# Performance work log

Measured on AMD Instinct MI355X. Metric: run time of the kernel, lower is better.

Reference implementation:

```python
import jax, jax.numpy as jnp
import numpy as np

EMB_DIM = 512
CATE1_CNT = 10
VOCAB = 100000
H_D = 1024
BN_EPS = 1e-5
NEG = -1e30  # masked value for max-pool


def setup_inputs() -> dict:
    key = jax.random.key(0)
    ks = jax.random.split(key, 12)
    B, LT, LD = 1024, 50, 200
    title = jax.random.randint(ks[0], (B, LT), 0, VOCAB, dtype=jnp.int64)
    desc = jax.random.randint(ks[1], (B, LD), 0, VOCAB, dtype=jnp.int64)
    t_len = jax.random.randint(ks[2], (B,), 1, LT + 1, dtype=jnp.int64)
    d_len = jax.random.randint(ks[3], (B,), 1, LD + 1, dtype=jnp.int64)
    emb = jax.random.normal(ks[4], (VOCAB, EMB_DIM), dtype=jnp.float32) * 0.02
    W_fc = jax.random.normal(ks[5], (4 * EMB_DIM, H_D), dtype=jnp.float32) * (1.0 / np.sqrt(4 * EMB_DIM))
    b_fc = jnp.zeros((H_D,), dtype=jnp.float32)
    gamma = jnp.ones((H_D,), dtype=jnp.float32)
    beta = jnp.zeros((H_D,), dtype=jnp.float32)
    W_clf = jax.random.normal(ks[6], (H_D, CATE1_CNT), dtype=jnp.float32) * (1.0 / np.sqrt(H_D))
    b_clf = jnp.zeros((CATE1_CNT,), dtype=jnp.float32)
    return {"title": title, "desc": desc, "t_len": t_len, "d_len": d_len,
            "emb": emb, "W_fc": W_fc, "b_fc": b_fc, "gamma": gamma,
            "beta": beta, "W_clf": W_clf, "b_clf": b_clf}


def _swem_pool(tokens, lens, emb):
    # tokens: [B, L] int, lens: [B] int -> (avg, max) each [B, D]
    e = emb[tokens]                                   # [B, L, D] gather
    L = tokens.shape[1]
    mask = (jnp.arange(L)[None, :] < lens[:, None])[..., None]  # [B, L, 1]
    s = jnp.sum(jnp.where(mask, e, 0.0), axis=1)      # [B, D]
    avg = s / jnp.maximum(lens, 1).astype(e.dtype)[:, None]
    mx = jnp.max(jnp.where(mask, e, NEG), axis=1)     # [B, D]
    return avg, mx


def reference(title, desc, t_len, d_len, emb, W_fc, b_fc, gamma, beta, W_clf, b_clf):
    t_avg, t_max = _swem_pool(title, t_len, emb)
    d_avg, d_max = _swem_pool(desc, d_len, emb)
    swem = jnp.concatenate([t_avg, t_max, d_avg, d_max], axis=-1)  # [B, 2048]
    h = swem @ W_fc + b_fc                                         # [B, H_D]
    # BatchNorm1d in training mode: batch statistics
    mean = jnp.mean(h, axis=0)
    var = jnp.var(h, axis=0)
    h = (h - mean) * jax.lax.rsqrt(var + BN_EPS) * gamma + beta
    h = jax.nn.relu(h)
    return h @ W_clf + b_clf                                       # [B, 10]
```

## Files before the change

### kernel.cpp

```cpp
#include <hip/hip_runtime.h>
#include <hip/hip_bf16.h>

#define EMB_DIM 512
#define B_SZ 1024
#define LT 50
#define LD 200
#define H_D 1024
#define K_FC 2048
#define NCLS 10
#define BN_EPS 1e-5f
#define NEGV -1e30f

typedef short short8 __attribute__((ext_vector_type(8)));
typedef float f32x4 __attribute__((ext_vector_type(4)));

#define SWZ(r, b) ((b) ^ (((r) & 7) << 4))

#define ACC4(S, M, E) \
  S.x += E.x; S.y += E.y; S.z += E.z; S.w += E.w; \
  M.x = fmaxf(M.x, E.x); M.y = fmaxf(M.y, E.y); \
  M.z = fmaxf(M.z, E.z); M.w = fmaxf(M.w, E.w);

__global__ __launch_bounds__(512) void pool_tr_kernel(
    const int* __restrict__ title, const int* __restrict__ desc,
    const int* __restrict__ t_len, const int* __restrict__ d_len,
    const float* __restrict__ emb, __hip_bfloat16* __restrict__ swem,
    const float* __restrict__ W, __hip_bfloat16* __restrict__ Wt) {
  __shared__ float sm[8192];
  __shared__ int idxs[264];

  const int bid = blockIdx.x;
  const int tid = threadIdx.x;

  if (bid >= 2 * B_SZ) {
    const int t = bid - 2 * B_SZ;
    const int n0 = (t & 15) * 64;
    const int k0 = (t >> 4) * 64;
#pragma unroll
    for (int i = 0; i < 8; ++i) {
      int idx = i * 512 + tid;
      int r = idx >> 6, c = idx & 63;
      sm[r * 65 + c] = W[(size_t)(k0 + r) * H_D + n0 + c];
    }
    __syncthreads();
#pragma unroll
    for (int i = 0; i < 8; ++i) {
      int idx = i * 512 + tid;
      int r = idx >> 6, c = idx & 63;
      Wt[(size_t)(n0 + r) * K_FC + k0 + c] = __float2bfloat16(sm[c * 65 + r]);
    }
    return;
  }

  const int b = bid >> 1;
  const int half = bid & 1;
  const int wave = tid >> 6;
  const int lane = tid & 63;
  const int dbase = half * 256 + lane * 4;

  if (tid < LT) idxs[tid] = title[b * LT + tid];
  else if (tid >= 64 && tid < 64 + LD) idxs[tid] = desc[b * LD + tid - 64];
  const int tl = t_len[b];
  const int dl = d_len[b];
  __syncthreads();

#define POOL_LIST(LEN, IDXOFF, SARR, MARR)                                         \
  {                                                                                \
    float4 s0 = make_float4(0.f, 0.f, 0.f, 0.f), s1 = s0;                          \
    float4 m0 = make_float4(NEGV, NEGV, NEGV, NEGV), m1 = m0;                      \
    const int cnt = (LEN > wave) ? ((LEN - wave + 7) >> 3) : 0;                    \
    if (cnt >= 2) {                                                                \
      float4 e0 = *reinterpret_cast<const float4*>(                                \
          emb + (size_t)idxs[IDXOFF + wave] * EMB_DIM + dbase);                    \
      float4 e1 = *reinterpret_cast<const float4*>(                                \
          emb + (size_t)idxs[IDXOFF + wave + 8] * EMB_DIM + dbase);                \
      int i = 2;                                                                   \
      for (; i + 1 < cnt; i += 2) {                                                \
        float4 n0 = *reinterpret_cast<const float4*>(                              \
            emb + (size_t)idxs[IDXOFF + wave + i * 8] * EMB_DIM + dbase);          \
        float4 n1 = *reinterpret_cast<const float4*>(                              \
            emb + (size_t)idxs[IDXOFF + wave + (i + 1) * 8] * EMB_DIM + dbase);    \
        ACC4(s0, m0, e0); ACC4(s1, m1, e1);                                        \
        e0 = n0; e1 = n1;                                                          \
      }                                                                            \
      ACC4(s0, m0, e0); ACC4(s1, m1, e1);                                          \
      if (i < cnt) {                                                               \
        float4 t2 = *reinterpret_cast<const float4*>(                              \
            emb + (size_t)idxs[IDXOFF + wave + i * 8] * EMB_DIM + dbase);          \
        ACC4(s0, m0, t2);                                                          \
      }                                                                            \
    } else if (cnt == 1) {                                                         \
      float4 e0 = *reinterpret_cast<const float4*>(                                \
          emb + (size_t)idxs[IDXOFF + wave] * EMB_DIM + dbase);                    \
      ACC4(s0, m0, e0);                                                            \
    }                                                                              \
    s0.x += s1.x; s0.y += s1.y; s0.z += s1.z; s0.w += s1.w;                        \
    m0.x = fmaxf(m0.x, m1.x); m0.y = fmaxf(m0.y, m1.y);                            \
    m0.z = fmaxf(m0.z, m1.z); m0.w = fmaxf(m0.w, m1.w);                            \
    *reinterpret_cast<float4*>(&sm[(SARR * 8 + wave) * 256 + lane * 4]) = s0;      \
    *reinterpret_cast<float4*>(&sm[(MARR * 8 + wave) * 256 + lane * 4]) = m0;      \
  }

  POOL_LIST(tl, 0, 0, 1)
  POOL_LIST(dl, 64, 2, 3)

  __syncthreads();

  if (tid < 64) {
    const float it = 1.0f / (float)tl;
    const float id = 1.0f / (float)dl;
    float4 ts = make_float4(0.f, 0.f, 0.f, 0.f);
    float4 tm = make_float4(NEGV, NEGV, NEGV, NEGV);
    float4 ds = make_float4(0.f, 0.f, 0.f, 0.f);
    float4 dm = make_float4(NEGV, NEGV, NEGV, NEGV);
#pragma unroll
    for (int w = 0; w < 8; ++w) {
      float4 a = *reinterpret_cast<const float4*>(&sm[(0 * 8 + w) * 256 + tid * 4]);
      ts.x += a.x; ts.y += a.y; ts.z += a.z; ts.w += a.w;
      float4 bmx = *reinterpret_cast<const float4*>(&sm[(1 * 8 + w) * 256 + tid * 4]);
      tm.x = fmaxf(tm.x, bmx.x); tm.y = fmaxf(tm.y, bmx.y);
      tm.z = fmaxf(tm.z, bmx.z); tm.w = fmaxf(tm.w, bmx.w);
      float4 c = *reinterpret_cast<const float4*>(&sm[(2 * 8 + w) * 256 + tid * 4]);
      ds.x += c.x; ds.y += c.y; ds.z += c.z; ds.w += c.w;
      float4 dmx = *reinterpret_cast<const float4*>(&sm[(3 * 8 + w) * 256 + tid * 4]);
      dm.x = fmaxf(dm.x, dmx.x); dm.y = fmaxf(dm.y, dmx.y);
      dm.z = fmaxf(dm.z, dmx.z); dm.w = fmaxf(dm.w, dmx.w);
    }
    __hip_bfloat16* row = swem + (size_t)b * K_FC + half * 256 + tid * 4;
    union { ushort4 v; __hip_bfloat16 h[4]; } u;
    u.h[0] = __float2bfloat16(ts.x * it); u.h[1] = __float2bfloat16(ts.y * it);
    u.h[2] = __float2bfloat16(ts.z * it); u.h[3] = __float2bfloat16(ts.w * it);
    *reinterpret_cast<ushort4*>(&row[0 * EMB_DIM]) = u.v;
    u.h[0] = __float2bfloat16(tm.x); u.h[1] = __float2bfloat16(tm.y);
    u.h[2] = __float2bfloat16(tm.z); u.h[3] = __float2bfloat16(tm.w);
    *reinterpret_cast<ushort4*>(&row[1 * EMB_DIM]) = u.v;
    u.h[0] = __float2bfloat16(ds.x * id); u.h[1] = __float2bfloat16(ds.y * id);
    u.h[2] = __float2bfloat16(ds.z * id); u.h[3] = __float2bfloat16(ds.w * id);
    *reinterpret_cast<ushort4*>(&row[2 * EMB_DIM]) = u.v;
    u.h[0] = __float2bfloat16(dm.x); u.h[1] = __float2bfloat16(dm.y);
    u.h[2] = __float2bfloat16(dm.z); u.h[3] = __float2bfloat16(dm.w);
    *reinterpret_cast<ushort4*>(&row[3 * EMB_DIM]) = u.v;
  }
}

__global__ __launch_bounds__(256) void gemm_mfma_kernel(
    const __hip_bfloat16* __restrict__ A,
    const __hip_bfloat16* __restrict__ Bt,
    const float* __restrict__ bias, float* __restrict__ C,
    float* __restrict__ psum, float* __restrict__ psq) {
  __shared__ unsigned char As[8192];
  __shared__ unsigned char Bs[8192];
  __shared__ float reds[2][2][2][16];
  __shared__ float redq[2][2][2][16];
  const int tid = threadIdx.x;
  const int lane = tid & 63;
  const int wave = tid >> 6;
  const int wr = wave >> 1, wc = wave & 1;
  const int m0 = blockIdx.y * 64, n0 = blockIdx.x * 64;

  f32x4 acc[2][2] = {};

  const int c0 = tid * 2, c1 = tid * 2 + 1;
  const int r0s = c0 >> 3, o0 = c0 & 7;
  const int r1s = c1 >> 3, o1 = c1 & 7;
  const int hi = lane >> 4;
  const int lo = lane & 15;

  for (int k0 = 0; k0 < K_FC; k0 += 64) {
    float4 a0 = *reinterpret_cast<const float4*>(A + (size_t)(m0 + r0s) * K_FC + k0 + o0 * 8);
    float4 a1 = *reinterpret_cast<const float4*>(A + (size_t)(m0 + r1s) * K_FC + k0 + o1 * 8);
    float4 b0 = *reinterpret_cast<const float4*>(Bt + (size_t)(n0 + r0s) * K_FC + k0 + o0 * 8);
    float4 b1 = *reinterpret_cast<const float4*>(Bt + (size_t)(n0 + r1s) * K_FC + k0 + o1 * 8);
    __syncthreads();
    *reinterpret_cast<float4*>(As + SWZ(r0s, r0s * 128 + o0 * 16)) = a0;
    *reinterpret_cast<float4*>(As + SWZ(r1s, r1s * 128 + o1 * 16)) = a1;
    *reinterpret_cast<float4*>(Bs + SWZ(r0s, r0s * 128 + o0 * 16)) = b0;
    *reinterpret_cast<float4*>(Bs + SWZ(r1s, r1s * 128 + o1 * 16)) = b1;
    __syncthreads();

#pragma unroll
    for (int kks = 0; kks < 2; ++kks) {
      short8 af[2], bfr[2];
#pragma unroll
      for (int mi = 0; mi < 2; ++mi) {
        int r = wr * 32 + mi * 16 + lo;
        af[mi] = *reinterpret_cast<const short8*>(As + SWZ(r, r * 128 + kks * 64 + hi * 16));
      }
#pragma unroll
      for (int ni = 0; ni < 2; ++ni) {
        int r = wc * 32 + ni * 16 + lo;
        bfr[ni] = *reinterpret_cast<const short8*>(Bs + SWZ(r, r * 128 + kks * 64 + hi * 16));
      }
#pragma unroll
      for (int mi = 0; mi < 2; ++mi)
#pragma unroll
        for (int ni = 0; ni < 2; ++ni)
          acc[mi][ni] = __builtin_amdgcn_mfma_f32_16x16x32_bf16(af[mi], bfr[ni], acc[mi][ni], 0, 0, 0);
    }
  }

#pragma unroll
  for (int ni = 0; ni < 2; ++ni) {
    int col = n0 + wc * 32 + ni * 16 + lo;
    float bv = bias[col];
    float s = 0.f, q = 0.f;
#pragma unroll
    for (int mi = 0; mi < 2; ++mi) {
#pragma unroll
      for (int r = 0; r < 4; ++r) {
        float v = acc[mi][ni][r] + bv;
        s += v; q += v * v;
        int rowm = m0 + wr * 32 + mi * 16 + hi * 4 + r;
        C[(size_t)rowm * H_D + col] = v;
      }
    }
    s += __shfl_xor(s, 16);
    s += __shfl_xor(s, 32);
    q += __shfl_xor(q, 16);
    q += __shfl_xor(q, 32);
    if (lane < 16) { reds[wr][wc][ni][lo] = s; redq[wr][wc][ni][lo] = q; }
  }
  __syncthreads();
  if (tid < 64) {
    int wc2 = tid >> 5, ni2 = (tid >> 4) & 1, lo2 = tid & 15;
    float s = reds[0][wc2][ni2][lo2] + reds[1][wc2][ni2][lo2];
    float q = redq[0][wc2][ni2][lo2] + redq[1][wc2][ni2][lo2];
    psum[blockIdx.y * H_D + n0 + tid] = s;
    psq[blockIdx.y * H_D + n0 + tid] = q;
  }
}

__global__ __launch_bounds__(256) void bn_final_kernel(
    const float* __restrict__ psum, const float* __restrict__ psq,
    const float* __restrict__ gamma, const float* __restrict__ beta,
    float* __restrict__ scale, float* __restrict__ shift) {
  const int col = blockIdx.x * 256 + threadIdx.x;
  float s = 0.f, q = 0.f;
#pragma unroll
  for (int i = 0; i < 16; ++i) {
    s += psum[i * H_D + col];
    q += psq[i * H_D + col];
  }
  const float inv_n = 1.0f / (float)B_SZ;
  float mean = s * inv_n;
  float var = q * inv_n - mean * mean;
  float rstd = rsqrtf(var + BN_EPS);
  float sc = rstd * gamma[col];
  scale[col] = sc;
  shift[col] = beta[col] - mean * sc;
}

__global__ __launch_bounds__(256) void clf_kernel(
    const float* __restrict__ h, const float* __restrict__ scale,
    const float* __restrict__ shift, const float* __restrict__ W,
    const float* __restrict__ bclf, float* __restrict__ out) {
  const int row = blockIdx.x;
  const int tid = threadIdx.x;
  float acc[NCLS] = {};
  for (int k = tid; k < H_D; k += 256) {
    float v = h[(size_t)row * H_D + k] * scale[k] + shift[k];
    v = fmaxf(v, 0.f);
    const float* w = &W[(size_t)k * NCLS];
#pragma unroll
    for (int j = 0; j < NCLS; ++j) acc[j] += v * w[j];
  }
#pragma unroll
  for (int j = 0; j < NCLS; ++j) {
    float v = acc[j];
#pragma unroll
    for (int off = 32; off > 0; off >>= 1) v += __shfl_down(v, off, 64);
    acc[j] = v;
  }
  __shared__ float part[4][NCLS];
  const int wave = tid >> 6;
  const int lane = tid & 63;
  if (lane == 0) {
#pragma unroll
    for (int j = 0; j < NCLS; ++j) part[wave][j] = acc[j];
  }
  __syncthreads();
  if (tid < NCLS) {
    float s = part[0][tid] + part[1][tid] + part[2][tid] + part[3][tid] + bclf[tid];
    out[(size_t)row * NCLS + tid] = s;
  }
}

extern "C" void kernel_launch(void* const* d_in, const int* in_sizes, int n_in,
                              void* d_out, int out_size, void* d_ws, size_t ws_size,
                              hipStream_t stream) {
  const int* title = (const int*)d_in[0];
  const int* desc  = (const int*)d_in[1];
  const int* t_len = (const int*)d_in[2];
  const int* d_len = (const int*)d_in[3];
  const float* emb   = (const float*)d_in[4];
  const float* W_fc  = (const float*)d_in[5];
  const float* b_fc  = (const float*)d_in[6];
  const float* gamma = (const float*)d_in[7];
  const float* beta  = (const float*)d_in[8];
  const float* W_clf = (const float*)d_in[9];
  const float* b_clf = (const float*)d_in[10];
  float* out = (float*)d_out;

  unsigned char* ws = (unsigned char*)d_ws;
  __hip_bfloat16* swem = (__hip_bfloat16*)ws;
  __hip_bfloat16* Wt   = (__hip_bfloat16*)(ws + (4u << 20));
  float* h     = (float*)(ws + (8u << 20));
  float* psum  = (float*)(ws + (12u << 20));
  float* psq   = psum + 16 * H_D;
  float* scale = psq + 16 * H_D;
  float* shift = scale + H_D;

  const int n_tr_blocks = (K_FC / 64) * (H_D / 64);
  pool_tr_kernel<<<2 * B_SZ + n_tr_blocks, 512, 0, stream>>>(
      title, desc, t_len, d_len, emb, swem, W_fc, Wt);
  gemm_mfma_kernel<<<dim3(H_D / 64, B_SZ / 64), 256, 0, stream>>>(swem, Wt, b_fc, h, psum, psq);
  bn_final_kernel<<<H_D / 256, 256, 0, stream>>>(psum, psq, gamma, beta, scale, shift);
  clf_kernel<<<B_SZ, 256, 0, stream>>>(h, scale, shift, W_clf, b_clf, out);
}
```

Measured before the change: 77.80 us.

## Register-prefetch next GEMM tile and transpose classifier weights for coalesced dot

The GEMM main loop now issues global loads for the next K-tile into registers right after the LDS store barrier, so the loads overlap the MFMA work on the current tile instead of stalling at the start of each iteration. Separately, the classifier weight is transposed once by an extra block in the pool/transpose kernel. The classifier kernel now stages the ReLU'd activations in shared memory and has each wave compute whole class dot products with coalesced weight reads. This removes the strided 10-wide weight reads and the ten-way shuffle reduction, at the cost of an extra block and slightly more register pressure in the GEMM.

```diff
diff --git a/kernel.cpp b/kernel.cpp
--- a/kernel.cpp
+++ b/kernel.cpp
@@ -25,7 +25,8 @@
     const int* __restrict__ title, const int* __restrict__ desc,
     const int* __restrict__ t_len, const int* __restrict__ d_len,
     const float* __restrict__ emb, __hip_bfloat16* __restrict__ swem,
-    const float* __restrict__ W, __hip_bfloat16* __restrict__ Wt) {
+    const float* __restrict__ W, __hip_bfloat16* __restrict__ Wt,
+    const float* __restrict__ Wclf, float* __restrict__ WclfT) {
   __shared__ float sm[8192];
   __shared__ int idxs[264];
 
@@ -34,6 +35,13 @@
 
   if (bid >= 2 * B_SZ) {
     const int t = bid - 2 * B_SZ;
+    if (t == 512) {
+      for (int idx = tid; idx < NCLS * H_D; idx += 512) {
+        int j = idx >> 10, k = idx & 1023;
+        WclfT[j * H_D + k] = Wclf[(size_t)k * NCLS + j];
+      }
+      return;
+    }
     const int n0 = (t & 15) * 64;
     const int k0 = (t >> 4) * 64;
 #pragma unroll
@@ -166,17 +174,30 @@
   const int hi = lane >> 4;
   const int lo = lane & 15;
 
+  const __hip_bfloat16* pa0 = A + (size_t)(m0 + r0s) * K_FC + o0 * 8;
+  const __hip_bfloat16* pa1 = A + (size_t)(m0 + r1s) * K_FC + o1 * 8;
+  const __hip_bfloat16* pb0 = Bt + (size_t)(n0 + r0s) * K_FC + o0 * 8;
+  const __hip_bfloat16* pb1 = Bt + (size_t)(n0 + r1s) * K_FC + o1 * 8;
+
+  float4 a0 = *reinterpret_cast<const float4*>(pa0);
+  float4 a1 = *reinterpret_cast<const float4*>(pa1);
+  float4 b0 = *reinterpret_cast<const float4*>(pb0);
+  float4 b1 = *reinterpret_cast<const float4*>(pb1);
+
   for (int k0 = 0; k0 < K_FC; k0 += 64) {
-    float4 a0 = *reinterpret_cast<const float4*>(A + (size_t)(m0 + r0s) * K_FC + k0 + o0 * 8);
-    float4 a1 = *reinterpret_cast<const float4*>(A + (size_t)(m0 + r1s) * K_FC + k0 + o1 * 8);
-    float4 b0 = *reinterpret_cast<const float4*>(Bt + (size_t)(n0 + r0s) * K_FC + k0 + o0 * 8);
-    float4 b1 = *reinterpret_cast<const float4*>(Bt + (size_t)(n0 + r1s) * K_FC + k0 + o1 * 8);
     __syncthreads();
     *reinterpret_cast<float4*>(As + SWZ(r0s, r0s * 128 + o0 * 16)) = a0;
     *reinterpret_cast<float4*>(As + SWZ(r1s, r1s * 128 + o1 * 16)) = a1;
     *reinterpret_cast<float4*>(Bs + SWZ(r0s, r0s * 128 + o0 * 16)) = b0;
     *reinterpret_cast<float4*>(Bs + SWZ(r1s, r1s * 128 + o1 * 16)) = b1;
     __syncthreads();
+
+    if (k0 + 64 < K_FC) {
+      a0 = *reinterpret_cast<const float4*>(pa0 + k0 + 64);
+      a1 = *reinterpret_cast<const float4*>(pa1 + k0 + 64);
+      b0 = *reinterpret_cast<const float4*>(pb0 + k0 + 64);
+      b1 = *reinterpret_cast<const float4*>(pb1 + k0 + 64);
+    }
 
 #pragma unroll
     for (int kks = 0; kks < 2; ++kks) {
@@ -252,36 +273,30 @@
 
 __global__ __launch_bounds__(256) void clf_kernel(
     const float* __restrict__ h, const float* __restrict__ scale,
-    const float* __restrict__ shift, const float* __restrict__ W,
+    const float* __restrict__ shift, const float* __restrict__ WT,
     const float* __restrict__ bclf, float* __restrict__ out) {
+  __shared__ float v[H_D];
   const int row = blockIdx.x;
   const int tid = threadIdx.x;
-  float acc[NCLS] = {};
-  for (int k = tid; k < H_D; k += 256) {
-    float v = h[(size_t)row * H_D + k] * scale[k] + shift[k];
-    v = fmaxf(v, 0.f);
-    const float* w = &W[(size_t)k * NCLS];
-#pragma unroll
-    for (int j = 0; j < NCLS; ++j) acc[j] += v * w[j];
-  }
-#pragma unroll
-  for (int j = 0; j < NCLS; ++j) {
-    float v = acc[j];
-#pragma unroll
-    for (int off = 32; off > 0; off >>= 1) v += __shfl_down(v, off, 64);
-    acc[j] = v;
-  }
-  __shared__ float part[4][NCLS];
-  const int wave = tid >> 6;
-  const int lane = tid & 63;
-  if (lane == 0) {
-#pragma unroll
-    for (int j = 0; j < NCLS; ++j) part[wave][j] = acc[j];
+#pragma unroll
+  for (int i = 0; i < 4; ++i) {
+    int k = tid + i * 256;
+    float x = h[(size_t)row * H_D + k] * scale[k] + shift[k];
+    v[k] = fmaxf(x, 0.f);
   }
   __syncthreads();
-  if (tid < NCLS) {
-    float s = part[0][tid] + part[1][tid] + part[2][tid] + part[3][tid] + bclf[tid];
-    out[(size_t)row * NCLS + tid] = s;
+  const int wave = tid >> 6, lane = tid & 63;
+  for (int j = wave; j < NCLS; j += 4) {
+    const float* wrow = WT + j * H_D;
+    float acc = 0.f;
+#pragma unroll
+    for (int i = 0; i < 16; ++i) {
+      int k = lane + i * 64;
+      acc += v[k] * wrow[k];
+    }
+#pragma unroll
+    for (int off = 32; off > 0; off >>= 1) acc += __shfl_down(acc, off, 64);
+    if (lane == 0) out[(size_t)row * NCLS + j] = acc + bclf[j];
   }
 }
 
@@ -309,11 +324,12 @@
   float* psq   = psum + 16 * H_D;
   float* scale = psq + 16 * H_D;
   float* shift = scale + H_D;
-
-  const int n_tr_blocks = (K_FC / 64) * (H_D / 64);
+  float* WclfT = shift + H_D;
+
+  const int n_tr_blocks = (K_FC / 64) * (H_D / 64) + 1;
   pool_tr_kernel<<<2 * B_SZ + n_tr_blocks, 512, 0, stream>>>(
-      title, desc, t_len, d_len, emb, swem, W_fc, Wt);
+      title, desc, t_len, d_len, emb, swem, W_fc, Wt, W_clf, WclfT);
   gemm_mfma_kernel<<<dim3(H_D / 64, B_SZ / 64), 256, 0, stream>>>(swem, Wt, b_fc, h, psum, psq);
   bn_final_kernel<<<H_D / 256, 256, 0, stream>>>(psum, psq, gamma, beta, scale, shift);
-  clf_kernel<<<B_SZ, 256, 0, stream>>>(h, scale, shift, W_clf, b_clf, out);
-}
+  clf_kernel<<<B_SZ, 256, 0, stream>>>(h, scale, shift, WclfT, b_clf, out);
+}
```

Result: faster. 74.29 us (-4.5%).
